# Kernel tuning notes

Measured on AMD Instinct MI355X. Metric: run time of the kernel, lower is better.

Reference implementation:

```python
import jax, jax.numpy as jnp
import numpy as np

L = 16          # num_layers
BLOCK_SIZE = 4  # commit partial block every BLOCK_SIZE layers
EPS_RMS = 1e-8
EPS_LN = 1e-5


def _rmsnorm(x):
    # RMSNorm without learned scale (matches source: x * rsqrt(mean(x^2) + eps))
    return x * jax.lax.rsqrt(jnp.mean(x * x, axis=-1, keepdims=True) + EPS_RMS)


def _layer_fn(x, g, b, W1, b1, W2, b2):
    # LayerNorm (affine) -> Linear(d,2d) -> GELU(exact) -> Linear(2d,d)
    mu = jnp.mean(x, axis=-1, keepdims=True)
    var = jnp.mean((x - mu) ** 2, axis=-1, keepdims=True)
    xn = (x - mu) * jax.lax.rsqrt(var + EPS_LN) * g + b
    h = jax.nn.gelu(xn @ W1 + b1, approximate=False)
    return h @ W2 + b2


def setup_inputs() -> dict:
    key = jax.random.key(0)
    ks = jax.random.split(key, 4)
    B, T, D = 8, 8192, 128
    return {
        "embedding": jax.random.normal(ks[0], (B, T, D), dtype=jnp.float32),
        "w": jax.random.normal(ks[1], (L, D), dtype=jnp.float32) * 0.02,
        "ln_g": jnp.ones((L, D), dtype=jnp.float32),
        "ln_b": jnp.zeros((L, D), dtype=jnp.float32),
        "W1": jax.random.normal(ks[2], (L, D, 2 * D), dtype=jnp.float32) * 0.02,
        "b1": jnp.zeros((L, 2 * D), dtype=jnp.float32),
        "W2": jax.random.normal(ks[3], (L, 2 * D, D), dtype=jnp.float32) * 0.02,
        "b2": jnp.zeros((L, D), dtype=jnp.float32),
    }


def reference(embedding, w, ln_g, ln_b, W1, b1, W2, b2):
    blocks = [embedding]
    partial = None
    h = embedding
    for l in range(L):
        sources = blocks + ([partial] if partial is not None else [])
        V = jnp.stack(sources)                       # [n, B, T, D] (n grows with l)
        K = _rmsnorm(V)
        logits = jnp.einsum('d,nbtd->nbt', w[l], K)  # [n, B, T]
        weights = jax.nn.softmax(logits, axis=0)     # softmax over block dim n
        h = jnp.einsum('nbt,nbtd->btd', weights, V)  # [B, T, D]
        v = _layer_fn(h, ln_g[l], ln_b[l], W1[l], b1[l], W2[l], b2[l])
        partial = v if partial is None else partial + v
        if (l + 1) % BLOCK_SIZE == 0:
            blocks.append(partial)
            partial = None
    return h
```

## Files before the change

### kernel.cpp

```cpp
#include <hip/hip_runtime.h>
#include <math.h>


typedef float    f32x4  __attribute__((ext_vector_type(4)));
typedef __bf16   bf16x8 __attribute__((ext_vector_type(8)));
typedef unsigned short u16x8 __attribute__((ext_vector_type(8)));

#define D 128

__device__ __forceinline__ unsigned short f2bf(float f) {
  unsigned int u = __builtin_bit_cast(unsigned int, f);
  u += 0x7fffu + ((u >> 16) & 1u);
  return (unsigned short)(u >> 16);
}

__device__ __forceinline__ float dot4(f32x4 a, f32x4 b) {
  return a.x * b.x + a.y * b.y + a.z * b.z + a.w * b.w;
}

__device__ __forceinline__ float fast_gelu(float x) {
  float y = fabsf(x) * 0.70710678118654752f;
  float t = 1.0f / fmaf(0.47047f, y, 1.0f);
  float P = fmaf(fmaf(0.7478556f, t, -0.0958798f), t, 0.3480242f) * t;
  float E = __expf(-y * y);
  float er = fmaf(-P, E, 1.0f);
  er = copysignf(er, x);
  return 0.5f * x * (1.0f + er);
}

__global__ __launch_bounds__(256) void pack_weights(
    const float* __restrict__ W1, const float* __restrict__ W2,
    unsigned short* __restrict__ W1p, unsigned short* __restrict__ W2p)
{
  int t = blockIdx.x * 256 + threadIdx.x;
  if (t < 16 * 128 * 256) {
    int layer = t >> 15, r = t & 32767;
    int j = r & 7, lane = (r >> 3) & 63, nt = (r >> 9) & 15, kk = (r >> 13) & 3;
    int k = kk * 32 + ((lane >> 4) << 3) + j;
    int n = (nt << 4) + (lane & 15);
    W1p[t] = f2bf(W1[(layer << 15) + (k << 8) + n]);
  } else {
    int t2 = t - 16 * 128 * 256;
    int layer = t2 >> 15, r = t2 & 32767;
    int j = r & 7, lane = (r >> 3) & 63, nt = (r >> 9) & 7, kk = (r >> 12) & 7;
    int k = kk * 32 + ((lane >> 4) << 3) + j;
    int n = (nt << 4) + (lane & 15);
    W2p[t2] = f2bf(W2[(layer << 15) + (k << 7) + n]);
  }
}

template<int NS, bool LAST>
__global__ __launch_bounds__(256) __attribute__((amdgpu_waves_per_eu(2)))
void fused4(const float* __restrict__ S0, const float* __restrict__ S1,
            const float* __restrict__ S2, const float* __restrict__ S3,
            const float* __restrict__ wv_all, const float* __restrict__ lng_all,
            const float* __restrict__ lnb_all,
            const unsigned short* __restrict__ W1p, const float* __restrict__ b1_all,
            const unsigned short* __restrict__ W2p, const float* __restrict__ b2_all,
            float* __restrict__ dst)
{
  __shared__ u16x8 A1f[2 * 4 * 64];
  __shared__ u16x8 A2f[2 * 8 * 64];
  __shared__ float SC[32 * 132];

  const int tid   = threadIdx.x;
  const int w     = tid >> 6;
  const int l     = tid & 63;
  const int tk8   = l >> 3;
  const int c8    = l & 7;
  const int r_blk = w * 8 + tk8;
  const int c0    = c8 * 16;
  const int tok   = blockIdx.x * 32 + r_blk;
  const int m_own = r_blk >> 4;
  const int row16 = r_blk & 15;
  const int ln15  = l & 15, lhi = l >> 4;

  unsigned short* A2u = (unsigned short*)A2f;
  const float* srcs[4] = {S0, S1, S2, S3};

  f32x4 V[NS][4];
  float rinv[NS];
  #pragma unroll
  for (int s = 0; s < NS; ++s) {
    const float* vp = srcs[s] + (size_t)tok * D + c0;
    float q = 0.f;
    #pragma unroll
    for (int i = 0; i < 4; ++i) {
      V[s][i] = *(const f32x4*)(vp + 4 * i);
      q += dot4(V[s][i], V[s][i]);
    }
    q += __shfl_xor(q, 1); q += __shfl_xor(q, 2); q += __shfl_xor(q, 4);
    rinv[s] = rsqrtf(q * (1.f / 128.f) + 1e-8f);
  }

  f32x4 part[4];
  #pragma unroll
  for (int i = 0; i < 4; ++i) part[i] = f32x4{0.f, 0.f, 0.f, 0.f};

  const int L0 = (NS - 1) * 4;

  #pragma unroll 1
  for (int ll = 0; ll < 4; ++ll) {
    const int layer = L0 + ll;

    const float* wl = wv_all + layer * D + c0;
    f32x4 wv[4];
    #pragma unroll
    for (int i = 0; i < 4; ++i) wv[i] = *(const f32x4*)(wl + 4 * i);

    float denom = 0.f;
    f32x4 hacc[4];
    #pragma unroll
    for (int i = 0; i < 4; ++i) hacc[i] = f32x4{0.f, 0.f, 0.f, 0.f};

    #pragma unroll
    for (int s = 0; s < NS; ++s) {
      float d2 = 0.f;
      #pragma unroll
      for (int i = 0; i < 4; ++i) d2 += dot4(wv[i], V[s][i]);
      d2 += __shfl_xor(d2, 1); d2 += __shfl_xor(d2, 2); d2 += __shfl_xor(d2, 4);
      float e = __expf(d2 * rinv[s]);
      denom += e;
      #pragma unroll
      for (int i = 0; i < 4; ++i) hacc[i] += e * V[s][i];
    }
    if (ll > 0) {
      float q = 0.f, d2 = 0.f;
      #pragma unroll
      for (int i = 0; i < 4; ++i) {
        q  += dot4(part[i], part[i]);
        d2 += dot4(wv[i], part[i]);
      }
      q  += __shfl_xor(q, 1);  q  += __shfl_xor(q, 2);  q  += __shfl_xor(q, 4);
      d2 += __shfl_xor(d2, 1); d2 += __shfl_xor(d2, 2); d2 += __shfl_xor(d2, 4);
      float rp = rsqrtf(q * (1.f / 128.f) + 1e-8f);
      float e = __expf(d2 * rp);
      denom += e;
      #pragma unroll
      for (int i = 0; i < 4; ++i) hacc[i] += e * part[i];
    }
    float inv = 1.0f / denom;
    #pragma unroll
    for (int i = 0; i < 4; ++i) hacc[i] *= inv;

    if (LAST && ll == 3) {
      float* op = dst + (size_t)tok * D + c0;
      #pragma unroll
      for (int i = 0; i < 4; ++i) *(f32x4*)(op + 4 * i) = hacc[i];
      return;
    }

    float sm = 0.f;
    #pragma unroll
    for (int i = 0; i < 4; ++i) sm += hacc[i].x + hacc[i].y + hacc[i].z + hacc[i].w;
    sm += __shfl_xor(sm, 1); sm += __shfl_xor(sm, 2); sm += __shfl_xor(sm, 4);
    float mu = sm * (1.f / 128.f);
    float sv = 0.f;
    #pragma unroll
    for (int i = 0; i < 4; ++i) {
      f32x4 d4 = hacc[i] - mu;
      sv += dot4(d4, d4);
    }
    sv += __shfl_xor(sv, 1); sv += __shfl_xor(sv, 2); sv += __shfl_xor(sv, 4);
    float rs = rsqrtf(sv * (1.f / 128.f) + 1e-5f);

    const float* gl = lng_all + layer * D + c0;
    const float* bl = lnb_all + layer * D + c0;
    f32x4 xn[4];
    #pragma unroll
    for (int i = 0; i < 4; ++i) {
      f32x4 g4 = *(const f32x4*)(gl + 4 * i);
      f32x4 b4 = *(const f32x4*)(bl + 4 * i);
      xn[i] = (hacc[i] - mu) * rs * g4 + b4;
    }
    {
      u16x8 pk0, pk1;
      pk0[0]=f2bf(xn[0].x); pk0[1]=f2bf(xn[0].y); pk0[2]=f2bf(xn[0].z); pk0[3]=f2bf(xn[0].w);
      pk0[4]=f2bf(xn[1].x); pk0[5]=f2bf(xn[1].y); pk0[6]=f2bf(xn[1].z); pk0[7]=f2bf(xn[1].w);
      pk1[0]=f2bf(xn[2].x); pk1[1]=f2bf(xn[2].y); pk1[2]=f2bf(xn[2].z); pk1[3]=f2bf(xn[2].w);
      pk1[4]=f2bf(xn[3].x); pk1[5]=f2bf(xn[3].y); pk1[6]=f2bf(xn[3].z); pk1[7]=f2bf(xn[3].w);
      int kk  = c8 >> 1;
      int hi0 = (c8 & 1) * 2;
      int FL0 = hi0 * 16 + row16, FL1 = (hi0 + 1) * 16 + row16;
      A1f[(m_own * 4 + kk) * 64 + (FL0 ^ kk)] = pk0;
      A1f[(m_own * 4 + kk) * 64 + (FL1 ^ kk)] = pk1;
    }
    __syncthreads();

    const u16x8* W1f = (const u16x8*)(W1p + (size_t)layer * 32768);
    const float* b1l = b1_all + layer * 256;
    const f32x4 z4 = {0.f, 0.f, 0.f, 0.f};
    #pragma unroll
    for (int q = 0; q < 4; ++q) {
      const int nt = q * 4 + w;
      bf16x8 bf[4];
      #pragma unroll
      for (int kk = 0; kk < 4; ++kk)
        bf[kk] = __builtin_bit_cast(bf16x8, W1f[(kk * 16 + nt) * 64 + l]);
      const float bb1 = b1l[nt * 16 + ln15];
      const int kk2 = nt >> 1;
      const int hi2 = ((nt & 1) << 1) + (ln15 >> 3);
      #pragma unroll
      for (int m = 0; m < 2; ++m) {
        f32x4 a = z4;
        #pragma unroll
        for (int kk = 0; kk < 4; ++kk) {
          bf16x8 af = __builtin_bit_cast(bf16x8, A1f[(m * 4 + kk) * 64 + (l ^ kk)]);
          a = __builtin_amdgcn_mfma_f32_16x16x32_bf16(af, bf[kk], a, 0, 0, 0);
        }
        #pragma unroll
        for (int r4 = 0; r4 < 4; ++r4) {
          float g = fast_gelu(a[r4] + bb1);
          int FL = hi2 * 16 + lhi * 4 + r4;
          A2u[(((m * 8 + kk2) * 64) + (FL ^ kk2)) * 8 + (l & 7)] = f2bf(g);
        }
      }
    }
    __syncthreads();

    const u16x8* W2f = (const u16x8*)(W2p + (size_t)layer * 32768);
    const float* b2l = b2_all + layer * D;
    #pragma unroll
    for (int p = 0; p < 2; ++p) {
      const int nt2 = p * 4 + w;
      bf16x8 bf[8];
      #pragma unroll
      for (int k2 = 0; k2 < 8; ++k2)
        bf[k2] = __builtin_bit_cast(bf16x8, W2f[(k2 * 8 + nt2) * 64 + l]);
      const int n = nt2 * 16 + ln15;
      const float bb2 = b2l[n];
      const int phys = (n & 96) + ((n + ((n >> 5) << 3)) & 31);
      #pragma unroll
      for (int m = 0; m < 2; ++m) {
        f32x4 a = z4;
        #pragma unroll
        for (int k2 = 0; k2 < 8; ++k2) {
          bf16x8 af = __builtin_bit_cast(bf16x8, A2f[(m * 8 + k2) * 64 + (l ^ k2)]);
          a = __builtin_amdgcn_mfma_f32_16x16x32_bf16(af, bf[k2], a, 0, 0, 0);
        }
        #pragma unroll
        for (int r4 = 0; r4 < 4; ++r4)
          SC[(m * 16 + lhi * 4 + r4) * 132 + phys] = a[r4] + bb2;
      }
    }
    __syncthreads();

    #pragma unroll
    for (int i = 0; i < 4; ++i) {
      int c = c0 + 4 * i;
      part[i] += *(const f32x4*)(SC + r_blk * 132 + (c & 96) + ((c + ((c >> 5) << 3)) & 31));
    }
  }

  float* op = dst + (size_t)tok * D + c0;
  #pragma unroll
  for (int i = 0; i < 4; ++i) *(f32x4*)(op + 4 * i) = part[i];
}

extern "C" void kernel_launch(void* const* d_in, const int* in_sizes, int n_in,
                              void* d_out, int out_size, void* d_ws, size_t ws_size,
                              hipStream_t stream)
{
  const float* emb = (const float*)d_in[0];
  const float* wv  = (const float*)d_in[1];
  const float* lng = (const float*)d_in[2];
  const float* lnb = (const float*)d_in[3];
  const float* W1  = (const float*)d_in[4];
  const float* b1  = (const float*)d_in[5];
  const float* W2  = (const float*)d_in[6];
  const float* b2  = (const float*)d_in[7];
  float* out = (float*)d_out;

  const int tokens = in_sizes[0] / D;
  const size_t tbytes = (size_t)tokens * D * sizeof(float);

  char* wsb = (char*)d_ws;
  float* P0 = (float*)(wsb + 0 * tbytes);
  float* P1 = (float*)(wsb + 1 * tbytes);
  float* P2 = (float*)(wsb + 2 * tbytes);
  unsigned short* W1p = (unsigned short*)(wsb + 3 * tbytes);
  unsigned short* W2p = W1p + 16 * 128 * 256;

  pack_weights<<<(16 * 128 * 256 * 2) / 256, 256, 0, stream>>>(W1, W2, W1p, W2p);

  const int grid = tokens / 32;
  fused4<1, false><<<grid, 256, 0, stream>>>(emb, nullptr, nullptr, nullptr,
      wv, lng, lnb, W1p, b1, W2p, b2, P0);
  fused4<2, false><<<grid, 256, 0, stream>>>(emb, P0, nullptr, nullptr,
      wv, lng, lnb, W1p, b1, W2p, b2, P1);
  fused4<3, false><<<grid, 256, 0, stream>>>(emb, P0, P1, nullptr,
      wv, lng, lnb, W1p, b1, W2p, b2, P2);
  fused4<4, true ><<<grid, 256, 0, stream>>>(emb, P0, P1, P2,
      wv, lng, lnb, W1p, b1, W2p, b2, out);
}
```

Measured before the change: 886.3 us.

## Stream source blocks per layer instead of holding them in registers

Each layer now re-reads the committed source blocks from global memory, double-buffering one block ahead and recomputing the RMS norm, where before all sources and their inverse norms were held in registers for the whole kernel. The waves_per_eu(2) hint is dropped, which lets register pressure set occupancy. This trades extra global/L2 traffic and repeated norm math for lower register use and higher occupancy. A __syncthreads is also added after the shared-memory read at the end of each layer iteration.

```diff
diff --git a/kernel.cpp b/kernel.cpp
--- a/kernel.cpp
+++ b/kernel.cpp
@@ -50,7 +50,7 @@
 }
 
 template<int NS, bool LAST>
-__global__ __launch_bounds__(256) __attribute__((amdgpu_waves_per_eu(2)))
+__global__ __launch_bounds__(256)
 void fused4(const float* __restrict__ S0, const float* __restrict__ S1,
             const float* __restrict__ S2, const float* __restrict__ S3,
             const float* __restrict__ wv_all, const float* __restrict__ lng_all,
@@ -74,24 +74,10 @@
   const int m_own = r_blk >> 4;
   const int row16 = r_blk & 15;
   const int ln15  = l & 15, lhi = l >> 4;
+  const size_t toff = (size_t)tok * D + c0;
 
   unsigned short* A2u = (unsigned short*)A2f;
   const float* srcs[4] = {S0, S1, S2, S3};
-
-  f32x4 V[NS][4];
-  float rinv[NS];
-  #pragma unroll
-  for (int s = 0; s < NS; ++s) {
-    const float* vp = srcs[s] + (size_t)tok * D + c0;
-    float q = 0.f;
-    #pragma unroll
-    for (int i = 0; i < 4; ++i) {
-      V[s][i] = *(const f32x4*)(vp + 4 * i);
-      q += dot4(V[s][i], V[s][i]);
-    }
-    q += __shfl_xor(q, 1); q += __shfl_xor(q, 2); q += __shfl_xor(q, 4);
-    rinv[s] = rsqrtf(q * (1.f / 128.f) + 1e-8f);
-  }
 
   f32x4 part[4];
   #pragma unroll
@@ -113,16 +99,32 @@
     #pragma unroll
     for (int i = 0; i < 4; ++i) hacc[i] = f32x4{0.f, 0.f, 0.f, 0.f};
 
+    f32x4 cur[4], nxt[4];
+    #pragma unroll
+    for (int i = 0; i < 4; ++i) cur[i] = *(const f32x4*)(srcs[0] + toff + 4 * i);
+
     #pragma unroll
     for (int s = 0; s < NS; ++s) {
-      float d2 = 0.f;
-      #pragma unroll
-      for (int i = 0; i < 4; ++i) d2 += dot4(wv[i], V[s][i]);
+      if (s + 1 < NS) {
+        #pragma unroll
+        for (int i = 0; i < 4; ++i) nxt[i] = *(const f32x4*)(srcs[s + 1] + toff + 4 * i);
+      }
+      float q = 0.f, d2 = 0.f;
+      #pragma unroll
+      for (int i = 0; i < 4; ++i) {
+        q  += dot4(cur[i], cur[i]);
+        d2 += dot4(wv[i], cur[i]);
+      }
+      q  += __shfl_xor(q, 1);  q  += __shfl_xor(q, 2);  q  += __shfl_xor(q, 4);
       d2 += __shfl_xor(d2, 1); d2 += __shfl_xor(d2, 2); d2 += __shfl_xor(d2, 4);
-      float e = __expf(d2 * rinv[s]);
+      float e = __expf(d2 * rsqrtf(q * (1.f / 128.f) + 1e-8f));
       denom += e;
       #pragma unroll
-      for (int i = 0; i < 4; ++i) hacc[i] += e * V[s][i];
+      for (int i = 0; i < 4; ++i) hacc[i] += e * cur[i];
+      if (s + 1 < NS) {
+        #pragma unroll
+        for (int i = 0; i < 4; ++i) cur[i] = nxt[i];
+      }
     }
     if (ll > 0) {
       float q = 0.f, d2 = 0.f;
@@ -133,8 +135,7 @@
       }
       q  += __shfl_xor(q, 1);  q  += __shfl_xor(q, 2);  q  += __shfl_xor(q, 4);
       d2 += __shfl_xor(d2, 1); d2 += __shfl_xor(d2, 2); d2 += __shfl_xor(d2, 4);
-      float rp = rsqrtf(q * (1.f / 128.f) + 1e-8f);
-      float e = __expf(d2 * rp);
+      float e = __expf(d2 * rsqrtf(q * (1.f / 128.f) + 1e-8f));
       denom += e;
       #pragma unroll
       for (int i = 0; i < 4; ++i) hacc[i] += e * part[i];
@@ -144,7 +145,7 @@
     for (int i = 0; i < 4; ++i) hacc[i] *= inv;
 
     if (LAST && ll == 3) {
-      float* op = dst + (size_t)tok * D + c0;
+      float* op = dst + toff;
       #pragma unroll
       for (int i = 0; i < 4; ++i) *(f32x4*)(op + 4 * i) = hacc[i];
       return;
@@ -250,9 +251,10 @@
       int c = c0 + 4 * i;
       part[i] += *(const f32x4*)(SC + r_blk * 132 + (c & 96) + ((c + ((c >> 5) << 3)) & 31));
     }
+    __syncthreads();
   }
 
-  float* op = dst + (size_t)tok * D + c0;
+  float* op = dst + toff;
   #pragma unroll
   for (int i = 0; i < 4; ++i) *(f32x4*)(op + 4 * i) = part[i];
 }
```

Result: faster. 774.4 us (-12.6%).
